# Kernel optimization log

Measured on AMD Instinct MI355X. Metric: run time of the kernel, lower is better.

Reference implementation:

```python
import jax, jax.numpy as jnp
import numpy as np

N = 50000      # nodes
E = 1250000    # edges (avg degree 32)
D = 64         # in_channels == hidden_channels
L = 3          # num_layers
IMPROVED_FILL = 2.0  # GCNConv(improved=True) self-loop weight


def setup_inputs() -> dict:
    key = jax.random.key(0)
    ks = jax.random.split(key, 6)
    x = jax.random.normal(ks[0], (N, D), dtype=jnp.float32)
    edge_index = jax.random.randint(ks[1], (2, E), 0, N, dtype=jnp.int64)
    edge_weight = jax.random.uniform(ks[2], (E,), dtype=jnp.float32)
    Ws = jax.random.normal(ks[3], (L, D, D), dtype=jnp.float32) / np.sqrt(D).astype(np.float32)
    bs = jnp.zeros((L, D), dtype=jnp.float32)
    Wf = jax.random.normal(ks[4], (D, 1), dtype=jnp.float32) / np.sqrt(D).astype(np.float32)
    bf = jnp.zeros((1,), dtype=jnp.float32)
    return dict(x=x, edge_index=edge_index, edge_weight=edge_weight,
                Ws=Ws, bs=bs, Wf=Wf, bf=bf, prob=0)


def _gcn_norm(edge_index, edge_weight, n):
    # add self-loops with fill value 2.0 (improved=True)
    loop = jnp.arange(n, dtype=edge_index.dtype)
    row = jnp.concatenate([edge_index[0], loop])  # source nodes (x_j)
    col = jnp.concatenate([edge_index[1], loop])  # target nodes (aggregation)
    w = jnp.concatenate([edge_weight,
                         jnp.full((n,), IMPROVED_FILL, edge_weight.dtype)])
    deg = jax.ops.segment_sum(w, col, num_segments=n)
    dis = jnp.where(deg > 0, jax.lax.rsqrt(deg), 0.0)  # deg^{-1/2}, inf->0
    norm = dis[row] * w * dis[col]                      # [E+N]
    return row, col, norm


def reference(x, edge_index, edge_weight, Ws, bs, Wf, bf, prob):
    n = x.shape[0]
    # gcn_norm depends only on graph structure; compute once, reuse per layer
    row, col, norm = _gcn_norm(edge_index, edge_weight, n)
    for l in range(Ws.shape[0]):
        h = x @ Ws[l]                                  # [N, D] linear transform
        msg = h[row] * norm[:, None]                   # gather + per-edge scale
        agg = jax.ops.segment_sum(msg, col, num_segments=n)  # scatter-add
        x = jax.nn.relu(agg + bs[l])
    # F.dropout(x, p=prob) with prob=0 -> identity (inference)
    return x @ Wf + bf                                 # [N, 1]
```

## Files before the change

### kernel.cpp

```cpp
#include <hip/hip_runtime.h>
#include <hip/hip_bf16.h>

#define DCH 64
#define NB_CSR 256
#define MAXBINS 256

typedef __attribute__((ext_vector_type(8))) short bfrag;
typedef __attribute__((ext_vector_type(4))) float ffrag;

static __device__ __forceinline__ unsigned short f2bf(float f) {
    unsigned u = __float_as_uint(f);
    unsigned r = (u + 0x7fffu + ((u >> 16) & 1u)) >> 16;
    return (unsigned short)r;
}
static __device__ __forceinline__ float bf2f(unsigned short s) {
    return __uint_as_float(((unsigned)s) << 16);
}

__global__ __launch_bounds__(1024) void binc_k(const int* __restrict__ col,
                                               unsigned* __restrict__ blkcnt, int e) {
    __shared__ unsigned bins[MAXBINS];
    int B = blockIdx.x, tid = threadIdx.x;
    int chunk = (e + NB_CSR - 1) / NB_CSR;
    int beg = B * chunk, end = min(e, beg + chunk);
    if (tid < MAXBINS) bins[tid] = 0;
    __syncthreads();
    for (int i = beg + tid; i < end; i += 1024)
        atomicAdd(&bins[col[i] >> 8], 1u);
    __syncthreads();
    if (tid < MAXBINS) blkcnt[B * MAXBINS + tid] = bins[tid];
}

__global__ __launch_bounds__(64) void bincur1_k(const unsigned* __restrict__ blkcnt,
                                                unsigned* __restrict__ blkcur,
                                                unsigned* __restrict__ tot) {
    int j = blockIdx.x, lane = threadIdx.x;
    unsigned carry = 0;
#pragma unroll
    for (int c = 0; c < NB_CSR; c += 64) {
        unsigned v = blkcnt[(size_t)(c + lane) * MAXBINS + j];
        unsigned s = v;
#pragma unroll
        for (int off = 1; off < 64; off <<= 1) {
            unsigned t = __shfl_up(s, off);
            if (lane >= off) s += t;
        }
        blkcur[(size_t)(c + lane) * MAXBINS + j] = carry + s - v;
        carry += __shfl(s, 63);
    }
    if (lane == 0) tot[j] = carry;
}

__global__ __launch_bounds__(256) void bincur2_k(const unsigned* __restrict__ tot,
                                                 int* __restrict__ binbase,
                                                 int* __restrict__ ptr,
                                                 int nbins, int n, int e) {
    __shared__ int wtot[4];
    int tid = threadIdx.x, lane = tid & 63, w = tid >> 6;
    int v = (tid < nbins) ? (int)tot[tid] : 0;
    int s = v;
#pragma unroll
    for (int off = 1; off < 64; off <<= 1) {
        int t = __shfl_up(s, off);
        if (lane >= off) s += t;
    }
    if (lane == 63) wtot[w] = s;
    __syncthreads();
    if (tid == 0) {
        int r = 0;
#pragma unroll
        for (int k = 0; k < 4; ++k) { int t = wtot[k]; wtot[k] = r; r += t; }
    }
    __syncthreads();
    int excl = s - v + wtot[w];
    if (tid < nbins) binbase[tid] = excl;
    if (tid == 0) { binbase[nbins] = e; ptr[n] = e; }
}

__global__ __launch_bounds__(1024) void binfill_k(const int* __restrict__ row,
                                                  const int* __restrict__ col,
                                                  const float* __restrict__ ew,
                                                  const unsigned* __restrict__ blkcur,
                                                  const int* __restrict__ binbase,
                                                  uint2* __restrict__ rec, int e) {
    __shared__ unsigned cur[MAXBINS];
    int B = blockIdx.x, tid = threadIdx.x;
    int chunk = (e + NB_CSR - 1) / NB_CSR;
    int beg = B * chunk, end = min(e, beg + chunk);
    if (tid < MAXBINS) cur[tid] = blkcur[(size_t)B * MAXBINS + tid]
                                + (unsigned)binbase[tid];
    __syncthreads();
    for (int i = beg + tid; i < end; i += 1024) {
        int c = col[i];
        unsigned slot = atomicAdd(&cur[c >> 8], 1u);
        rec[slot] = make_uint2((unsigned)row[i] | ((unsigned)(c & 255) << 20),
                               __float_as_uint(ew[i]));
    }
}

__global__ __launch_bounds__(1024) void csr_k(const uint2* __restrict__ rec,
                                              const int* __restrict__ binbase,
                                              int* __restrict__ ptr,
                                              uint2* __restrict__ edg,
                                              float* __restrict__ dis, int n) {
    __shared__ unsigned ncnt[256];
    __shared__ unsigned nbase[256];
    __shared__ float degs[256];
    int b = blockIdx.x, tid = threadIdx.x;
    int beg = binbase[b], end = binbase[b + 1];
    int node0 = b << 8;
    int nn = min(256, n - node0);
    if (tid < 256) { ncnt[tid] = 0; degs[tid] = 0.f; }
    __syncthreads();
    for (int i = beg + tid; i < end; i += 1024) {
        uint2 r = rec[i];
        unsigned c8 = r.x >> 20;
        atomicAdd(&ncnt[c8], 1u);
        atomicAdd(&degs[c8], __uint_as_float(r.y));
    }
    __syncthreads();
    if (tid == 0) {
        unsigned run = (unsigned)beg;
        for (int k = 0; k < 256; ++k) { nbase[k] = run; run += ncnt[k]; }
    }
    __syncthreads();
    if (tid < nn) {
        ptr[node0 + tid] = (int)nbase[tid];
        dis[node0 + tid] = rsqrtf(degs[tid] + 2.0f);
    }
    if (tid < 256) ncnt[tid] = 0;
    __syncthreads();
    for (int i = beg + tid; i < end; i += 1024) {
        uint2 r = rec[i];
        unsigned c8 = r.x >> 20;
        unsigned pos = nbase[c8] + atomicAdd(&ncnt[c8], 1u);
        edg[pos] = make_uint2(r.x & 0xFFFFFu, r.y);
    }
}

__global__ __launch_bounds__(256) void normw_k(uint2* __restrict__ edg,
                                               const float* __restrict__ dis, int e) {
    int i = blockIdx.x * 256 + threadIdx.x;
    if (i >= e) return;
    uint2 ev = edg[i];
    ((unsigned*)edg)[2 * i + 1] =
        __float_as_uint(__uint_as_float(ev.y) * dis[ev.x]);
}

__global__ __launch_bounds__(256) void pack_k(const float* __restrict__ Ws,
                                              short* __restrict__ wpk, int L) {
    int ent = blockIdx.x * 256 + threadIdx.x;
    if (ent >= L * 512) return;
    int layer = ent >> 9;
    int r = ent & 511;
    int lane = r & 63;
    int st = r >> 6;
    int s = st >> 2, t = st & 3;
    int quad = lane >> 4;
    int ncol = t * 16 + (lane & 15);
    const float* W = Ws + (size_t)layer * DCH * DCH;
    union { short sh[8]; int4 v; } hi, lo;
#pragma unroll
    for (int j = 0; j < 8; ++j) {
        int k = s * 32 + quad * 8 + j;
        float w = W[k * DCH + ncol];
        unsigned short h = f2bf(w);
        hi.sh[j] = (short)h;
        lo.sh[j] = (short)f2bf(w - bf2f(h));
    }
    *(int4*)(wpk + ((size_t)(layer * 2 + 0) * 512 + r) * 8) = hi.v;
    *(int4*)(wpk + ((size_t)(layer * 2 + 1) * 512 + r) * 8) = lo.v;
}

__global__ __launch_bounds__(256) void gemm_k(const float* __restrict__ x,
                                              const short* __restrict__ wpk_layer,
                                              unsigned short* __restrict__ hb, int n_tiles) {
    __shared__ short Wl[2][512 * 8];
    {
        const int4* src = (const int4*)wpk_layer;
        int4* dst = (int4*)&Wl[0][0];
        for (int i = threadIdx.x; i < 1024; i += 256) dst[i] = src[i];
    }
    __syncthreads();
    int wave = threadIdx.x >> 6, lane = threadIdx.x & 63;
    int tile = blockIdx.x * 4 + wave;
    if (tile >= n_tiles) return;
    int m = lane & 15, quad = lane >> 4;
    int row = tile * 16 + m;

    float av[2][8];
    {
        const float4* p0 = (const float4*)(x + (size_t)row * DCH + quad * 8);
        const float4* p1 = (const float4*)(x + (size_t)row * DCH + 32 + quad * 8);
        float4 a0 = p0[0], a1 = p0[1], b0 = p1[0], b1 = p1[1];
        av[0][0] = a0.x; av[0][1] = a0.y; av[0][2] = a0.z; av[0][3] = a0.w;
        av[0][4] = a1.x; av[0][5] = a1.y; av[0][6] = a1.z; av[0][7] = a1.w;
        av[1][0] = b0.x; av[1][1] = b0.y; av[1][2] = b0.z; av[1][3] = b0.w;
        av[1][4] = b1.x; av[1][5] = b1.y; av[1][6] = b1.z; av[1][7] = b1.w;
    }
    bfrag ah[2], al[2];
#pragma unroll
    for (int s = 0; s < 2; ++s)
#pragma unroll
        for (int j = 0; j < 8; ++j) {
            unsigned short hbv = f2bf(av[s][j]);
            ah[s][j] = (short)hbv;
            al[s][j] = (short)f2bf(av[s][j] - bf2f(hbv));
        }

#pragma unroll
    for (int t = 0; t < 4; ++t) {
        ffrag acc = {0.f, 0.f, 0.f, 0.f};
#pragma unroll
        for (int s = 0; s < 2; ++s) {
            bfrag wh = *(bfrag*)&Wl[0][((s * 4 + t) * 64 + lane) * 8];
            bfrag wl = *(bfrag*)&Wl[1][((s * 4 + t) * 64 + lane) * 8];
            acc = __builtin_amdgcn_mfma_f32_16x16x32_bf16(ah[s], wh, acc, 0, 0, 0);
            acc = __builtin_amdgcn_mfma_f32_16x16x32_bf16(al[s], wh, acc, 0, 0, 0);
            acc = __builtin_amdgcn_mfma_f32_16x16x32_bf16(ah[s], wl, acc, 0, 0, 0);
        }
        int colc = t * 16 + m;
#pragma unroll
        for (int r = 0; r < 4; ++r)
            hb[(size_t)(tile * 16 + quad * 4 + r) * DCH + colc] = f2bf(acc[r]);
    }
}

static __device__ __forceinline__ void gather_node(int node, int lane, int p, int hf,
                                                   float dis_c,
                                                   const int* __restrict__ ptr,
                                                   const uint2* __restrict__ edg,
                                                   const unsigned* __restrict__ hbf,
                                                   float& A0, float& A1) {
    float a0 = 0.f, a1 = 0.f;
    if (hf == 0) {
        unsigned sv = hbf[(size_t)node * 32 + p];
        a0 = 2.0f * dis_c * __uint_as_float(sv << 16);
        a1 = 2.0f * dis_c * __uint_as_float(sv & 0xffff0000u);
    }
    int beg = ptr[node], end = ptr[node + 1];
    for (int base = beg; base < end; base += 64) {
        int idx = base + lane;
        int rv = 0; float nv = 0.f;
        if (idx < end) {
            uint2 ev = edg[idx];
            rv = (int)ev.x;
            nv = __uint_as_float(ev.y);
        }
        int m = min(64, end - base);
        int steps = (((m + 1) >> 1) + 15) & ~15;
        for (int j0 = 0; j0 < steps; j0 += 16) {
            unsigned hv[16]; float nn[16];
#pragma unroll
            for (int q = 0; q < 16; ++q) {
                int eidx = 2 * (j0 + q) + hf;
                int r = __shfl(rv, eidx);
                nn[q] = __shfl(nv, eidx);
                hv[q] = hbf[(size_t)r * 32 + p];
            }
#pragma unroll
            for (int q = 0; q < 16; ++q) {
                a0 += __uint_as_float(hv[q] << 16) * nn[q];
                a1 += __uint_as_float(hv[q] & 0xffff0000u) * nn[q];
            }
        }
    }
    A0 = a0 + __shfl_xor(a0, 32);
    A1 = a1 + __shfl_xor(a1, 32);
}

__global__ __launch_bounds__(256) void gg_k(const int* __restrict__ ptr,
                                            const uint2* __restrict__ edg,
                                            const float* __restrict__ dis,
                                            const unsigned* __restrict__ hbf,
                                            const float* __restrict__ b,
                                            const short* __restrict__ wpk_next,
                                            unsigned short* __restrict__ hb_out, int n) {
    __shared__ float xs[16][68];
    int w = threadIdx.x >> 6, lane = threadIdx.x & 63;
    int p = lane & 31, hf = lane >> 5;
    int tile = blockIdx.x;
    float2 bv = ((const float2*)b)[p];
#pragma unroll 1
    for (int i = 0; i < 4; ++i) {
        int node = tile * 16 + w * 4 + i;
        if (node < n) {
            float dis_c = dis[node];
            float A0, A1;
            gather_node(node, lane, p, hf, dis_c, ptr, edg, hbf, A0, A1);
            if (hf == 0) {
                xs[w * 4 + i][2 * p]     = fmaxf(dis_c * A0 + bv.x, 0.f);
                xs[w * 4 + i][2 * p + 1] = fmaxf(dis_c * A1 + bv.y, 0.f);
            }
        }
    }
    __syncthreads();
    int m = lane & 15, quad = lane >> 4, t = w;
    bfrag ah[2], al[2];
#pragma unroll
    for (int s = 0; s < 2; ++s)
#pragma unroll
        for (int j = 0; j < 8; ++j) {
            float v = xs[m][s * 32 + quad * 8 + j];
            unsigned short hbv = f2bf(v);
            ah[s][j] = (short)hbv;
            al[s][j] = (short)f2bf(v - bf2f(hbv));
        }
    ffrag acc = {0.f, 0.f, 0.f, 0.f};
#pragma unroll
    for (int s = 0; s < 2; ++s) {
        bfrag wh = *(const bfrag*)(wpk_next + ((size_t)((s * 4 + t) * 64 + lane)) * 8);
        bfrag wl = *(const bfrag*)(wpk_next + ((size_t)(512 + (s * 4 + t) * 64 + lane)) * 8);
        acc = __builtin_amdgcn_mfma_f32_16x16x32_bf16(ah[s], wh, acc, 0, 0, 0);
        acc = __builtin_amdgcn_mfma_f32_16x16x32_bf16(al[s], wh, acc, 0, 0, 0);
        acc = __builtin_amdgcn_mfma_f32_16x16x32_bf16(ah[s], wl, acc, 0, 0, 0);
    }
    int colc = t * 16 + m;
#pragma unroll
    for (int r = 0; r < 4; ++r) {
        int orow = tile * 16 + quad * 4 + r;
        if (orow < n) hb_out[(size_t)orow * DCH + colc] = f2bf(acc[r]);
    }
}

__global__ __launch_bounds__(256) void gf_k(const int* __restrict__ ptr,
                                            const uint2* __restrict__ edg,
                                            const float* __restrict__ dis,
                                            const unsigned* __restrict__ hbf,
                                            const float* __restrict__ b,
                                            const float* __restrict__ Wf,
                                            const float* __restrict__ bf,
                                            float* __restrict__ out, int n) {
    int node = blockIdx.x * 4 + (threadIdx.x >> 6);
    int lane = threadIdx.x & 63;
    if (node >= n) return;
    int p = lane & 31, hf = lane >> 5;
    float dis_c = dis[node];
    float A0, A1;
    gather_node(node, lane, p, hf, dis_c, ptr, edg, hbf, A0, A1);
    float2 bv = ((const float2*)b)[p];
    float2 wv = ((const float2*)Wf)[p];
    float x0 = fmaxf(dis_c * A0 + bv.x, 0.f);
    float x1 = fmaxf(dis_c * A1 + bv.y, 0.f);
    float v = x0 * wv.x + x1 * wv.y;
#pragma unroll
    for (int off = 16; off > 0; off >>= 1) v += __shfl_down(v, off);
    if (lane == 0) out[node] = v + bf[0];
}

extern "C" void kernel_launch(void* const* d_in, const int* in_sizes, int n_in,
                              void* d_out, int out_size, void* d_ws, size_t ws_size,
                              hipStream_t stream) {
    const float* x0 = (const float*)d_in[0];
    const int*   ei = (const int*)d_in[1];
    const float* ew = (const float*)d_in[2];
    const float* Ws = (const float*)d_in[3];
    const float* bs = (const float*)d_in[4];
    const float* Wf = (const float*)d_in[5];
    const float* bf = (const float*)d_in[6];

    const int n = in_sizes[0] / DCH;
    const int e = in_sizes[2];
    const int L = in_sizes[3] / (DCH * DCH);

    const int* row = ei;
    const int* col = ei + e;
    const int nbins = (n + 255) >> 8;

    size_t off = 0;
    auto alloc = [&](size_t bytes) {
        off = (off + 255) & ~(size_t)255;
        void* r = (char*)d_ws + off;
        off += bytes;
        return r;
    };
    int*      ptr     = (int*)     alloc((size_t)(n + 1) * 4);
    float*    dis     = (float*)   alloc((size_t)n * 4);
    short*    wpk     = (short*)   alloc((size_t)L * 2 * 512 * 8 * 2);
    uint2*    edg     = (uint2*)   alloc((size_t)e * 8);
    unsigned* blkcnt  = (unsigned*)alloc((size_t)NB_CSR * MAXBINS * 4);
    unsigned* blkcur  = (unsigned*)alloc((size_t)NB_CSR * MAXBINS * 4);
    unsigned* tot     = (unsigned*)alloc((size_t)MAXBINS * 4);
    int*      binbase = (int*)     alloc((size_t)(MAXBINS + 1) * 4);
    size_t szR = (size_t)e * 8;
    size_t szH = (size_t)2 * n * DCH * 2;
    unsigned char* regA = (unsigned char*)alloc(szR > szH ? szR : szH);
    uint2* rec = (uint2*)regA;
    unsigned short* hb_a = (unsigned short*)regA;
    unsigned short* hb_b = hb_a + (size_t)n * DCH;

    dim3 blk(256);
    const int n_tiles = (n + 15) / 16;

    binc_k   <<<dim3(NB_CSR), dim3(1024), 0, stream>>>(col, blkcnt, e);
    bincur1_k<<<dim3(nbins), dim3(64), 0, stream>>>(blkcnt, blkcur, tot);
    bincur2_k<<<dim3(1), blk, 0, stream>>>(tot, binbase, ptr, nbins, n, e);
    binfill_k<<<dim3(NB_CSR), dim3(1024), 0, stream>>>(row, col, ew, blkcur, binbase, rec, e);
    csr_k    <<<dim3(nbins), dim3(1024), 0, stream>>>(rec, binbase, ptr, edg, dis, n);
    normw_k  <<<dim3((e + 255) / 256), blk, 0, stream>>>(edg, dis, e);
    pack_k   <<<dim3((L * 512 + 255) / 256), blk, 0, stream>>>(Ws, wpk, L);

    const size_t wstride = (size_t)2 * 512 * 8;
    gemm_k<<<dim3((n_tiles + 3) / 4), blk, 0, stream>>>(x0, wpk, hb_a, n_tiles);
    gg_k  <<<dim3(n_tiles), blk, 0, stream>>>(ptr, edg, dis, (const unsigned*)hb_a,
                                              bs, wpk + wstride, hb_b, n);
    gg_k  <<<dim3(n_tiles), blk, 0, stream>>>(ptr, edg, dis, (const unsigned*)hb_b,
                                              bs + DCH, wpk + 2 * wstride, hb_a, n);
    gf_k  <<<dim3((n + 3) / 4), blk, 0, stream>>>(ptr, edg, dis, (const unsigned*)hb_a,
                                                  bs + 2 * DCH, Wf, bf, (float*)d_out, n);
}
```

Baseline: 221.0 us.

## Widen gather to 8-byte loads with four edges per wave, parallelize bin scan

The neighbor gather now has each lane load 4 bf16 channels (uint2) instead of 2. A wave therefore covers a 64-channel row with 16 lanes and processes four edges at once instead of two, and the partial sums are reduced across lane groups with xor shuffles. This halves the number of load instructions per gathered row and the per-edge shuffle overhead, at the cost of more accumulator registers and a two-stage reduction. Separately, the serial single-thread prefix sum over 256 bin counts in CSR build is replaced with a wave-level shuffle scan.

```diff
diff --git a/kernel.cpp b/kernel.cpp
--- a/kernel.cpp
+++ b/kernel.cpp
@@ -119,9 +119,20 @@
         atomicAdd(&degs[c8], __uint_as_float(r.y));
     }
     __syncthreads();
-    if (tid == 0) {
-        unsigned run = (unsigned)beg;
-        for (int k = 0; k < 256; ++k) { nbase[k] = run; run += ncnt[k]; }
+    if (tid < 64) {
+        unsigned carry = (unsigned)beg;
+#pragma unroll
+        for (int c = 0; c < 256; c += 64) {
+            unsigned v = ncnt[c + tid];
+            unsigned s = v;
+#pragma unroll
+            for (int off = 1; off < 64; off <<= 1) {
+                unsigned t = __shfl_up(s, off);
+                if (tid >= off) s += t;
+            }
+            nbase[c + tid] = carry + s - v;
+            carry += __shfl(s, 63);
+        }
     }
     __syncthreads();
     if (tid < nn) {
@@ -226,17 +237,20 @@
     }
 }
 
-static __device__ __forceinline__ void gather_node(int node, int lane, int p, int hf,
+static __device__ __forceinline__ void gather_node(int node, int lane, int pp, int eo,
                                                    float dis_c,
                                                    const int* __restrict__ ptr,
                                                    const uint2* __restrict__ edg,
                                                    const unsigned* __restrict__ hbf,
-                                                   float& A0, float& A1) {
-    float a0 = 0.f, a1 = 0.f;
-    if (hf == 0) {
-        unsigned sv = hbf[(size_t)node * 32 + p];
-        a0 = 2.0f * dis_c * __uint_as_float(sv << 16);
-        a1 = 2.0f * dis_c * __uint_as_float(sv & 0xffff0000u);
+                                                   float a[4]) {
+    a[0] = a[1] = a[2] = a[3] = 0.f;
+    if (eo == 0) {
+        uint2 sv = *(const uint2*)(hbf + (size_t)node * 32 + 2 * pp);
+        float wsl = 2.0f * dis_c;
+        a[0] = wsl * __uint_as_float(sv.x << 16);
+        a[1] = wsl * __uint_as_float(sv.x & 0xffff0000u);
+        a[2] = wsl * __uint_as_float(sv.y << 16);
+        a[3] = wsl * __uint_as_float(sv.y & 0xffff0000u);
     }
     int beg = ptr[node], end = ptr[node + 1];
     for (int base = beg; base < end; base += 64) {
@@ -248,25 +262,30 @@
             nv = __uint_as_float(ev.y);
         }
         int m = min(64, end - base);
-        int steps = (((m + 1) >> 1) + 15) & ~15;
-        for (int j0 = 0; j0 < steps; j0 += 16) {
-            unsigned hv[16]; float nn[16];
-#pragma unroll
-            for (int q = 0; q < 16; ++q) {
-                int eidx = 2 * (j0 + q) + hf;
+        int steps = (((m + 3) >> 2) + 7) & ~7;
+        for (int j0 = 0; j0 < steps; j0 += 8) {
+            uint2 hv[8]; float nn[8];
+#pragma unroll
+            for (int q = 0; q < 8; ++q) {
+                int eidx = 4 * (j0 + q) + eo;
                 int r = __shfl(rv, eidx);
                 nn[q] = __shfl(nv, eidx);
-                hv[q] = hbf[(size_t)r * 32 + p];
+                hv[q] = *(const uint2*)(hbf + (size_t)r * 32 + 2 * pp);
             }
 #pragma unroll
-            for (int q = 0; q < 16; ++q) {
-                a0 += __uint_as_float(hv[q] << 16) * nn[q];
-                a1 += __uint_as_float(hv[q] & 0xffff0000u) * nn[q];
+            for (int q = 0; q < 8; ++q) {
+                a[0] += __uint_as_float(hv[q].x << 16) * nn[q];
+                a[1] += __uint_as_float(hv[q].x & 0xffff0000u) * nn[q];
+                a[2] += __uint_as_float(hv[q].y << 16) * nn[q];
+                a[3] += __uint_as_float(hv[q].y & 0xffff0000u) * nn[q];
             }
         }
     }
-    A0 = a0 + __shfl_xor(a0, 32);
-    A1 = a1 + __shfl_xor(a1, 32);
+#pragma unroll
+    for (int j = 0; j < 4; ++j) {
+        a[j] += __shfl_xor(a[j], 16);
+        a[j] += __shfl_xor(a[j], 32);
+    }
 }
 
 __global__ __launch_bounds__(256) void gg_k(const int* __restrict__ ptr,
@@ -278,19 +297,23 @@
                                             unsigned short* __restrict__ hb_out, int n) {
     __shared__ float xs[16][68];
     int w = threadIdx.x >> 6, lane = threadIdx.x & 63;
-    int p = lane & 31, hf = lane >> 5;
+    int pp = lane & 15, eo = lane >> 4;
     int tile = blockIdx.x;
-    float2 bv = ((const float2*)b)[p];
+    float4 bv = ((const float4*)b)[pp];
 #pragma unroll 1
     for (int i = 0; i < 4; ++i) {
         int node = tile * 16 + w * 4 + i;
         if (node < n) {
             float dis_c = dis[node];
-            float A0, A1;
-            gather_node(node, lane, p, hf, dis_c, ptr, edg, hbf, A0, A1);
-            if (hf == 0) {
-                xs[w * 4 + i][2 * p]     = fmaxf(dis_c * A0 + bv.x, 0.f);
-                xs[w * 4 + i][2 * p + 1] = fmaxf(dis_c * A1 + bv.y, 0.f);
+            float a[4];
+            gather_node(node, lane, pp, eo, dis_c, ptr, edg, hbf, a);
+            if (eo == 0) {
+                float4 o;
+                o.x = fmaxf(dis_c * a[0] + bv.x, 0.f);
+                o.y = fmaxf(dis_c * a[1] + bv.y, 0.f);
+                o.z = fmaxf(dis_c * a[2] + bv.z, 0.f);
+                o.w = fmaxf(dis_c * a[3] + bv.w, 0.f);
+                *(float4*)&xs[w * 4 + i][4 * pp] = o;
             }
         }
     }
@@ -334,17 +357,18 @@
     int node = blockIdx.x * 4 + (threadIdx.x >> 6);
     int lane = threadIdx.x & 63;
     if (node >= n) return;
-    int p = lane & 31, hf = lane >> 5;
+    int pp = lane & 15, eo = lane >> 4;
     float dis_c = dis[node];
-    float A0, A1;
-    gather_node(node, lane, p, hf, dis_c, ptr, edg, hbf, A0, A1);
-    float2 bv = ((const float2*)b)[p];
-    float2 wv = ((const float2*)Wf)[p];
-    float x0 = fmaxf(dis_c * A0 + bv.x, 0.f);
-    float x1 = fmaxf(dis_c * A1 + bv.y, 0.f);
-    float v = x0 * wv.x + x1 * wv.y;
-#pragma unroll
-    for (int off = 16; off > 0; off >>= 1) v += __shfl_down(v, off);
+    float a[4];
+    gather_node(node, lane, pp, eo, dis_c, ptr, edg, hbf, a);
+    float4 bv = ((const float4*)b)[pp];
+    float4 wv = ((const float4*)Wf)[pp];
+    float v = fmaxf(dis_c * a[0] + bv.x, 0.f) * wv.x
+            + fmaxf(dis_c * a[1] + bv.y, 0.f) * wv.y
+            + fmaxf(dis_c * a[2] + bv.z, 0.f) * wv.z
+            + fmaxf(dis_c * a[3] + bv.w, 0.f) * wv.w;
+#pragma unroll
+    for (int off = 8; off > 0; off >>= 1) v += __shfl_xor(v, off);
     if (lane == 0) out[node] = v + bf[0];
 }
 
```

Result: faster. 209.0 us (-5.4%).
